# Performance work log

Hardware: AMD Instinct MI355X
Metric: run time of the kernel (lower is better)

Reference implementation:

```python
import jax, jax.numpy as jnp
import numpy as np

EPS = 1e-12


def setup_inputs() -> dict:
    key = jax.random.key(0)
    x = jax.random.normal(key, (32, 3000, 512), dtype=jnp.float32)
    return {"x": x, "kernel_size": 100}


def _window_sum(a, k):
    # sliding sum of length-k windows (stride 1) along axis 1; a: [B, Tpad, D] -> [B, Tpad-k+1, D]
    return jax.lax.reduce_window(a, 0.0, jax.lax.add, (1, k, 1), (1, 1, 1), 'VALID')


def reference(x, kernel_size):
    k = int(kernel_size)
    B, T, D = x.shape
    if T < k:
        # global CMVN fallback (torch.std default is unbiased, ddof=1)
        m = x.mean(axis=1, keepdims=True)
        v = x.std(axis=1, ddof=1, keepdims=True)
        return (x - m) / (v + EPS)
    # per-position effective window counts matching torch's denom construction:
    # ramp k//2..k-1, then k for the interior, then k-1 down to k//2
    denom = jnp.concatenate([
        jnp.arange(k // 2, k),
        jnp.full((T - k,), k),
        jnp.arange(k - 1, k // 2 - 1, -1),
    ]).astype(x.dtype)[None, :, None]  # [1, T, 1]
    # zero-pad time axis exactly like F.pad(..., (k//2, k//2 - 1))
    x_pad = jnp.pad(x, ((0, 0), (k // 2, k // 2 - 1), (0, 0)))
    s1 = _window_sum(x_pad, k)            # sum of window values (zeros at pads) [B, T, D]
    s2 = _window_sum(x_pad * x_pad, k)    # sum of squares                        [B, T, D]
    m = s1 / denom
    # torch sums (window - m)^2 over all k slots INCLUDING zero-padded slots:
    # sum (w - m)^2 = s2 - 2*m*s1 + k*m^2
    var_sum = s2 - 2.0 * m * s1 + k * m * m
    v = jnp.sqrt(var_sum / (k - 1))
    return (x - m) / (v + EPS)
```

## Files before the change

kernel.cpp:

```cpp
#include <hip/hip_runtime.h>

#define EPS 1e-12f


typedef float f4 __attribute__((ext_vector_type(4)));

constexpr int Bq = 32, Tq = 3000, Dq = 512;
constexpr int SEGR = 25;
constexpr int WT = 4;
constexpr int TB = SEGR * WT;
constexpr int NCHUNK = Tq / SEGR;
constexpr int NGRP = Tq / TB;
constexpr int NB = Bq * NGRP;
constexpr int NXCD = 8;
constexpr int NSEGL = WT + 3;

__global__ __launch_bounds__(512, 4) void mavn_kernel(
    const float* __restrict__ x, const int* __restrict__ kptr,
    float* __restrict__ out)
{
    __shared__ float lds1[NSEGL][Dq];
    __shared__ float lds2[NSEGL][Dq];

    const int g = blockIdx.x;
    const int xcd = g & (NXCD - 1);
    const int slot = g >> 3;
    const int pair = xcd * (NB / NXCD) + slot;
    const int b = pair / NGRP;
    const int grp = pair % NGRP;
    const int c0 = grp * WT;

    const int tid = threadIdx.x;
    const int w = tid >> 6;
    const int l = tid & 63;
    const int tw = w >> 1;
    const int dh = w & 1;

    const int k = kptr[0];
    const int half = k >> 1;

    const size_t bbase = (size_t)b * Tq * Dq;
    const int doff = dh * (Dq / 2) + l * 4;

    if (k == 4 * SEGR) {
        for (int tk = w; tk < 2 * NSEGL; tk += 8) {
            const int si = tk % NSEGL;
            const int sdh = tk / NSEGL;
            const int cs = c0 + si - 2;
            if (cs >= 0 && cs < NCHUNK) {
                const float* sp = x + bbase + (size_t)(cs * SEGR) * Dq
                                  + sdh * (Dq / 2) + l * 4;
                f4 a1 = {0.f, 0.f, 0.f, 0.f};
                f4 a2 = a1, c1 = a1, c2 = a1;
#pragma unroll 5
                for (int j = 0; j < SEGR; j += 2) {
                    const f4 v = *(const f4*)(sp + (size_t)j * Dq);
                    a1 += v; a2 += v * v;
                    if (j + 1 < SEGR) {
                        const f4 u = *(const f4*)(sp + (size_t)(j + 1) * Dq);
                        c1 += u; c2 += u * u;
                    }
                }
                ((f4*)&lds1[si][sdh * (Dq / 2)])[l] = a1 + c1;
                ((f4*)&lds2[si][sdh * (Dq / 2)])[l] = a2 + c2;
            }
        }
    }
    __syncthreads();

    const int c = c0 + tw;
    const int t0 = c * SEGR;
    const int t1 = t0 + SEGR;
    const float kf = (float)k;
    const float inv_km1 = 1.0f / (float)(k - 1);
    const int tail_start = Tq - (k - half);
    const float* xp = x + bbase + doff;
    float* op = out + bbase + doff;

    const bool interior = (k == 4 * SEGR) && (t0 >= half) &&
                          (t0 + SEGR - 1 + (k - half) - 1 <= Tq - 1) &&
                          (t0 + SEGR - 1 < tail_start);

    if (interior) {
        f4 s1 = {0.f, 0.f, 0.f, 0.f};
        f4 s2 = s1;
#pragma unroll
        for (int i = 0; i < 4; ++i) {
            s1 += ((const f4*)&lds1[tw + i][dh * (Dq / 2)])[l];
            s2 += ((const f4*)&lds2[tw + i][dh * (Dq / 2)])[l];
        }
        const float inv_k = 1.0f / kf;
        {
            const f4 xc = *(const f4*)(xp + (size_t)t0 * Dq);
            f4 o;
#pragma unroll
            for (int cc = 0; cc < 4; ++cc) {
                const float m = s1[cc] * inv_k;
                float var_sum = s2[cc] - m * s1[cc];
                var_sum = fmaxf(var_sum, 1e-12f);
                const float r = __builtin_amdgcn_rsqf(var_sum * inv_km1);
                o[cc] = (xc[cc] - m) * r;
            }
            __builtin_nontemporal_store(o, (f4*)(op + (size_t)t0 * Dq));
        }
        const int inoff = (k - half) - 1;
        const int oboff = -(half + 1);
        f4 n0 = *(const f4*)(xp + (size_t)(t0 + 1) * Dq);
        f4 n1 = *(const f4*)(xp + (size_t)(t0 + 2) * Dq);
        f4 i0 = *(const f4*)(xp + (size_t)(t0 + 1 + inoff) * Dq);
        f4 i1 = *(const f4*)(xp + (size_t)(t0 + 2 + inoff) * Dq);
        f4 o0 = *(const f4*)(xp + (size_t)(t0 + 1 + oboff) * Dq);
        f4 o1 = *(const f4*)(xp + (size_t)(t0 + 2 + oboff) * Dq);
        for (int j = 1; j < SEGR; j += 2) {
            const f4 cn0 = n0, cn1 = n1, ci0 = i0, ci1 = i1, co0 = o0, co1 = o1;
            {
                const int jn = (j + 2 <= SEGR - 2) ? j + 2 : j;
                n0 = *(const f4*)(xp + (size_t)(t0 + jn) * Dq);
                n1 = *(const f4*)(xp + (size_t)(t0 + jn + 1) * Dq);
                i0 = *(const f4*)(xp + (size_t)(t0 + jn + inoff) * Dq);
                i1 = *(const f4*)(xp + (size_t)(t0 + jn + 1 + inoff) * Dq);
                o0 = *(const f4*)(xp + (size_t)(t0 + jn + oboff) * Dq);
                o1 = *(const f4*)(xp + (size_t)(t0 + jn + 1 + oboff) * Dq);
            }
            s1 += ci0 - co0;
            s2 += ci0 * ci0 - co0 * co0;
            f4 oa;
#pragma unroll
            for (int cc = 0; cc < 4; ++cc) {
                const float m = s1[cc] * inv_k;
                float var_sum = s2[cc] - m * s1[cc];
                var_sum = fmaxf(var_sum, 1e-12f);
                const float r = __builtin_amdgcn_rsqf(var_sum * inv_km1);
                oa[cc] = (cn0[cc] - m) * r;
            }
            __builtin_nontemporal_store(oa, (f4*)(op + (size_t)(t0 + j) * Dq));
            s1 += ci1 - co1;
            s2 += ci1 * ci1 - co1 * co1;
            f4 ob;
#pragma unroll
            for (int cc = 0; cc < 4; ++cc) {
                const float m = s1[cc] * inv_k;
                float var_sum = s2[cc] - m * s1[cc];
                var_sum = fmaxf(var_sum, 1e-12f);
                const float r = __builtin_amdgcn_rsqf(var_sum * inv_km1);
                ob[cc] = (cn1[cc] - m) * r;
            }
            __builtin_nontemporal_store(ob, (f4*)(op + (size_t)(t0 + j + 1) * Dq));
        }
        return;
    }

    f4 s1 = {0.f, 0.f, 0.f, 0.f};
    f4 s2 = s1;
    {
        const int wlo = (t0 - half > 0) ? t0 - half : 0;
        const int whi = (t0 + (k - half) < Tq) ? t0 + (k - half) : Tq;
        f4 a1 = s1, a2 = s1;
        int j = wlo;
        for (; j + 1 < whi; j += 2) {
            const f4 v = *(const f4*)(xp + (size_t)j * Dq);
            const f4 u = *(const f4*)(xp + (size_t)(j + 1) * Dq);
            s1 += v; s2 += v * v;
            a1 += u; a2 += u * u;
        }
        if (j < whi) {
            const f4 v = *(const f4*)(xp + (size_t)j * Dq);
            s1 += v; s2 += v * v;
        }
        s1 += a1; s2 += a2;
    }

    f4 nx = *(const f4*)(xp + (size_t)t0 * Dq);
    f4 ia = {0.f, 0.f, 0.f, 0.f};
    f4 ob = ia;
    float wa = 0.f, wb = 0.f;

    for (int t = t0; t < t1; ++t) {
        const f4 cnum = nx;
        const f4 cin = ia;
        const f4 cout = ob;
        const float cwa = wa, cwb = wb;

        {
            const int tn = (t + 1 < t1) ? t + 1 : t;
            nx = *(const f4*)(xp + (size_t)tn * Dq);
            int ja = tn + (k - half) - 1;
            int jr = tn - half - 1;
            wa = (ja < Tq && tn > t0) ? 1.f : 0.f;
            wb = (jr >= 0 && tn > t0) ? 1.f : 0.f;
            ja = ja < Tq - 1 ? ja : Tq - 1; ja = ja > 0 ? ja : 0;
            jr = jr > 0 ? jr : 0;
            ia = *(const f4*)(xp + (size_t)ja * Dq);
            ob = *(const f4*)(xp + (size_t)jr * Dq);
        }

        s1 += cwa * cin - cwb * cout;
        s2 += cwa * cin * cin - cwb * cout * cout;

        int idn = half + t;
        idn = idn < k ? idn : k;
        const int tail = (k - 1) - (t - tail_start);
        idn = idn < tail ? idn : tail;
        const float inv_denom = __builtin_amdgcn_rcpf((float)idn);

        f4 o;
#pragma unroll
        for (int cc = 0; cc < 4; ++cc) {
            const float m = s1[cc] * inv_denom;
            float var_sum = s2[cc] - 2.0f * m * s1[cc] + kf * m * m;
            var_sum = fmaxf(var_sum, 0.0f);
            const float sd = __builtin_amdgcn_sqrtf(var_sum * inv_km1);
            o[cc] = (cnum[cc] - m) * __builtin_amdgcn_rcpf(sd + EPS);
        }
        __builtin_nontemporal_store(o, (f4*)(op + (size_t)t * Dq));
    }
}

extern "C" void kernel_launch(void* const* d_in, const int* in_sizes, int n_in,
                              void* d_out, int out_size, void* d_ws, size_t ws_size,
                              hipStream_t stream) {
    const float* x = (const float*)d_in[0];
    const int* kptr = (const int*)d_in[1];
    float* out = (float*)d_out;
    (void)in_sizes; (void)n_in; (void)out_size; (void)d_ws; (void)ws_size;

    mavn_kernel<<<NB, 512, 0, stream>>>(x, kptr, out);
}
```

Baseline: 113.2 us.

## Split segment-sum precompute into separate kernel writing to workspace

Moves the per-block computation of 25-row segment sums (sum and sum of squares) out of the main kernel into a dedicated pre-pass that writes them to a global workspace. The main kernel drops its LDS staging and __syncthreads, and reads four precomputed segment sums from the workspace to seed each interior window. Occupancy hint raised to 8 blocks per CU. The aim is to remove redundant overlapping segment reductions and the block barrier. The trade-off is an extra kernel launch and a full additional pass over the input, plus workspace traffic.

```diff
diff --git a/kernel.cpp b/kernel.cpp
--- a/kernel.cpp
+++ b/kernel.cpp
@@ -7,87 +7,88 @@
 
 constexpr int Bq = 32, Tq = 3000, Dq = 512;
 constexpr int SEGR = 25;
+constexpr int NSEG = Tq / SEGR;
 constexpr int WT = 4;
 constexpr int TB = SEGR * WT;
-constexpr int NCHUNK = Tq / SEGR;
 constexpr int NGRP = Tq / TB;
-constexpr int NB = Bq * NGRP;
+constexpr int NBm = Bq * NGRP;
 constexpr int NXCD = 8;
-constexpr int NSEGL = WT + 3;
-
-__global__ __launch_bounds__(512, 4) void mavn_kernel(
+
+__global__ __launch_bounds__(128) void seg_sums_kernel(
+    const float* __restrict__ x, float* __restrict__ ws)
+{
+    const int s = blockIdx.x;
+    const int b = blockIdx.y;
+    const int d4 = threadIdx.x;
+    const float* xp = x + ((size_t)b * Tq) * Dq + (size_t)d4 * 4;
+
+    f4 a1 = {0.f, 0.f, 0.f, 0.f};
+    f4 a2 = a1, b1 = a1, b2 = a1;
+    const int r0 = s * SEGR;
+#pragma unroll 5
+    for (int j = 0; j < SEGR; j += 2) {
+        const f4 v = *(const f4*)(xp + (size_t)(r0 + j) * Dq);
+        a1 += v; a2 += v * v;
+        if (j + 1 < SEGR) {
+            const f4 w = *(const f4*)(xp + (size_t)(r0 + j + 1) * Dq);
+            b1 += w; b2 += w * w;
+        }
+    }
+    f4* w1 = (f4*)ws;
+    f4* w2 = w1 + (size_t)Bq * NSEG * (Dq / 4);
+    const size_t idx = ((size_t)b * NSEG + s) * (Dq / 4) + d4;
+    w1[idx] = a1 + b1;
+    w2[idx] = a2 + b2;
+}
+
+__global__ __launch_bounds__(512, 8) void mavn_kernel(
     const float* __restrict__ x, const int* __restrict__ kptr,
-    float* __restrict__ out)
+    float* __restrict__ out, const float* __restrict__ ws, int use_seg)
 {
-    __shared__ float lds1[NSEGL][Dq];
-    __shared__ float lds2[NSEGL][Dq];
-
     const int g = blockIdx.x;
     const int xcd = g & (NXCD - 1);
     const int slot = g >> 3;
-    const int pair = xcd * (NB / NXCD) + slot;
+    const int pair = xcd * (NBm / NXCD) + slot;
     const int b = pair / NGRP;
     const int grp = pair % NGRP;
-    const int c0 = grp * WT;
 
     const int tid = threadIdx.x;
     const int w = tid >> 6;
     const int l = tid & 63;
-    const int tw = w >> 1;
+    const int q = w >> 1;
     const int dh = w & 1;
+
+    const int c = grp * WT + q;
+    const int t0 = c * SEGR;
+    const int t1 = t0 + SEGR;
 
     const int k = kptr[0];
     const int half = k >> 1;
-
     const size_t bbase = (size_t)b * Tq * Dq;
     const int doff = dh * (Dq / 2) + l * 4;
-
-    if (k == 4 * SEGR) {
-        for (int tk = w; tk < 2 * NSEGL; tk += 8) {
-            const int si = tk % NSEGL;
-            const int sdh = tk / NSEGL;
-            const int cs = c0 + si - 2;
-            if (cs >= 0 && cs < NCHUNK) {
-                const float* sp = x + bbase + (size_t)(cs * SEGR) * Dq
-                                  + sdh * (Dq / 2) + l * 4;
-                f4 a1 = {0.f, 0.f, 0.f, 0.f};
-                f4 a2 = a1, c1 = a1, c2 = a1;
-#pragma unroll 5
-                for (int j = 0; j < SEGR; j += 2) {
-                    const f4 v = *(const f4*)(sp + (size_t)j * Dq);
-                    a1 += v; a2 += v * v;
-                    if (j + 1 < SEGR) {
-                        const f4 u = *(const f4*)(sp + (size_t)(j + 1) * Dq);
-                        c1 += u; c2 += u * u;
-                    }
-                }
-                ((f4*)&lds1[si][sdh * (Dq / 2)])[l] = a1 + c1;
-                ((f4*)&lds2[si][sdh * (Dq / 2)])[l] = a2 + c2;
-            }
-        }
-    }
-    __syncthreads();
-
-    const int c = c0 + tw;
-    const int t0 = c * SEGR;
-    const int t1 = t0 + SEGR;
+    const float* xp = x + bbase + doff;
+    float* op = out + bbase + doff;
+
     const float kf = (float)k;
     const float inv_km1 = 1.0f / (float)(k - 1);
     const int tail_start = Tq - (k - half);
-    const float* xp = x + bbase + doff;
-    float* op = out + bbase + doff;
-
-    const bool interior = (k == 4 * SEGR) && (t0 >= half) &&
+
+    const bool seg_ok = use_seg && (k == 4 * SEGR);
+    const bool interior = seg_ok && (t0 >= half) &&
                           (t0 + SEGR - 1 + (k - half) - 1 <= Tq - 1) &&
                           (t0 + SEGR - 1 < tail_start);
 
     if (interior) {
+        const f4* w1 = (const f4*)ws;
+        const f4* w2 = w1 + (size_t)Bq * NSEG * (Dq / 4);
+        const int colf4 = dh * (Dq / 8) + l;
         f4 s1 = {0.f, 0.f, 0.f, 0.f};
         f4 s2 = s1;
 #pragma unroll
         for (int i = 0; i < 4; ++i) {
-            s1 += ((const f4*)&lds1[tw + i][dh * (Dq / 2)])[l];
-            s2 += ((const f4*)&lds2[tw + i][dh * (Dq / 2)])[l];
+            const size_t idx = ((size_t)b * NSEG + (c - 2 + i)) * (Dq / 4) + colf4;
+            s1 += w1[idx];
+            s2 += w2[idx];
         }
         const float inv_k = 1.0f / kf;
         {
@@ -136,16 +137,16 @@
             __builtin_nontemporal_store(oa, (f4*)(op + (size_t)(t0 + j) * Dq));
             s1 += ci1 - co1;
             s2 += ci1 * ci1 - co1 * co1;
-            f4 ob;
+            f4 ob2;
 #pragma unroll
             for (int cc = 0; cc < 4; ++cc) {
                 const float m = s1[cc] * inv_k;
                 float var_sum = s2[cc] - m * s1[cc];
                 var_sum = fmaxf(var_sum, 1e-12f);
                 const float r = __builtin_amdgcn_rsqf(var_sum * inv_km1);
-                ob[cc] = (cn1[cc] - m) * r;
-            }
-            __builtin_nontemporal_store(ob, (f4*)(op + (size_t)(t0 + j + 1) * Dq));
+                ob2[cc] = (cn1[cc] - m) * r;
+            }
+            __builtin_nontemporal_store(ob2, (f4*)(op + (size_t)(t0 + j + 1) * Dq));
         }
         return;
     }
@@ -222,7 +223,14 @@
     const float* x = (const float*)d_in[0];
     const int* kptr = (const int*)d_in[1];
     float* out = (float*)d_out;
-    (void)in_sizes; (void)n_in; (void)out_size; (void)d_ws; (void)ws_size;
-
-    mavn_kernel<<<NB, 512, 0, stream>>>(x, kptr, out);
+    (void)in_sizes; (void)n_in; (void)out_size;
+
+    const size_t ws_need = 2ull * Bq * NSEG * Dq * sizeof(float);
+    const int use_seg = (d_ws != nullptr && ws_size >= ws_need) ? 1 : 0;
+
+    if (use_seg) {
+        dim3 g1(NSEG, Bq);
+        seg_sums_kernel<<<g1, 128, 0, stream>>>(x, (float*)d_ws);
+    }
+    mavn_kernel<<<NBm, 512, 0, stream>>>(x, kptr, out, (const float*)d_ws, use_seg);
 }
```

Result: slower. 123.2 us (+8.8%).
